# Performance work log

Hardware: AMD Instinct MI355X
Metric: run time of the kernel (lower is better)

Reference implementation:

```python
import jax, jax.numpy as jnp
import numpy as np

N_NODES = 100000
N_EDGES = 1600000
MAX_RADIUS = 3.0
NUM_BASIS = 3
SQRT2 = 2.0 ** 0.5
# e3nn soft_one_hot_linspace 'smooth_finite' prefactor
C_SMOOTH = 1.14136 * float(np.exp(2.0))


def _sus(x):
    # smooth unit step: exp(-1/x) for x>0 else 0 (NaN-safe for grad)
    safe = jnp.where(x > 0.0, x, 1.0)
    return jnp.where(x > 0.0, jnp.exp(-1.0 / safe), 0.0)


def radial_embed(d):
    # soft_one_hot_linspace(d, 0, max_radius, 3, basis='smooth_finite', cutoff=True) * sqrt(num_basis)
    values = jnp.linspace(0.0, MAX_RADIUS, NUM_BASIS + 2)[1:-1]  # [3]
    step = MAX_RADIUS / (NUM_BASIS + 1)
    diff = (d[:, None] - values) / step  # [E,3]
    y = C_SMOOTH * _sus(diff + 1.0) * _sus(1.0 - diff)
    return y * (NUM_BASIS ** 0.5)


def fcnet(x, w1, w2):
    # e3nn FullyConnectedNet([3,16,numel], relu): normalized weights, normalize2mom(relu)=sqrt(2)*relu
    h = SQRT2 * jax.nn.relu(x @ (w1 / w1.shape[0] ** 0.5))
    return h @ (w2 / w2.shape[0] ** 0.5)


def reference(pos, feat, edge_src, edge_dst, fc1_w1, fc1_w2, core_w1, core_w2, fc3_w1, fc3_w2, conv_w, conv_b):
    n = pos.shape[0]
    z = edge_src.shape[0] / n  # average num neighbors
    edge_vec = pos[edge_dst] - pos[edge_src]
    d = jnp.sqrt(jnp.sum(edge_vec * edge_vec, axis=1))  # edges are self-loop-free -> d > 0
    emb = radial_embed(d)  # [E,3]

    # NOTE on e3nn math: with input/mid/output parities all even and sh = 0e+1o+2e,
    # the only parity-allowed paths producing nonzero output are the 0e (scalar) paths,
    # which contract against Y_0 = 1 ('component' normalization). The 4x1e block of the
    # mid irreps is identically zero (no parity-allowed path ever populates it), so the
    # math below (scalar block only, with e3nn path weights) is exactly equivalent.
    def conv(x, w1, w2, mul_in, mul_out, path_w):
        # per-edge weights from radial MLP; keep the 0e->0e instruction block
        w = fcnet(emb, w1, w2)[:, : mul_in * mul_out].reshape(-1, mul_in, mul_out)
        msg = path_w * jnp.einsum('euw,eu->ew', w, x[edge_src])
        return jax.ops.segment_sum(msg, edge_dst, num_segments=n) / z ** 0.5

    x = conv(feat, fc1_w1, fc1_w2, 3, 4, (1.0 / 3.0) ** 0.5)  # tp1: fan_in 3*1 -> pw=1/sqrt(3)
    for i in range(3):
        x = conv(x, core_w1[i], core_w2[i], 4, 4, 0.5)  # tp2 0e path: pw=sqrt(1/4)
    x = conv(x, fc3_w1, fc3_w2, 4, 16, 0.5)  # tp3: pw=sqrt(1/4)
    # Conv1d(16, 2, 1) == pointwise linear
    return x @ conv_w.T + conv_b


def setup_inputs():
    key = jax.random.key(0)
    ks = jax.random.split(key, 12)
    pos = jax.random.uniform(ks[0], (N_NODES, 3), dtype=jnp.float32)  # unit box -> all edge lengths < max_radius
    feat = jax.random.normal(ks[1], (N_NODES, 3), dtype=jnp.float32)
    edge_src = jax.random.randint(ks[2], (N_EDGES,), 0, N_NODES, dtype=jnp.int32)
    off = jax.random.randint(ks[3], (N_EDGES,), 1, N_NODES, dtype=jnp.int32)
    edge_dst = ((edge_src + off) % N_NODES).astype(jnp.int32)  # radius_graph has no self-loops
    return {
        'pos': pos,
        'feat': feat,
        'edge_src': edge_src,
        'edge_dst': edge_dst,
        'fc1_w1': jax.random.normal(ks[4], (3, 16), jnp.float32),
        'fc1_w2': jax.random.normal(ks[5], (16, 12), jnp.float32),
        'core_w1': jax.random.normal(ks[6], (3, 3, 16), jnp.float32),
        'core_w2': jax.random.normal(ks[7], (3, 16, 48), jnp.float32),
        'fc3_w1': jax.random.normal(ks[8], (3, 16), jnp.float32),
        'fc3_w2': jax.random.normal(ks[9], (16, 64), jnp.float32),
        'conv_w': jax.random.normal(ks[10], (2, 16), jnp.float32) * 0.25,
        'conv_b': jax.random.normal(ks[11], (2,), jnp.float32) * 0.1,
    }
```

## Files before the change

kernel.cpp:

```cpp
#include <hip/hip_runtime.h>


#define BCAP 4608
#define NBMAX 400

__device__ __forceinline__ float sus_f(float x) {
    return x > 0.0f ? __expf(-1.0f / x) : 0.0f;
}

__device__ __forceinline__ float uload(const float* p) {
    return __uint_as_float(__builtin_amdgcn_readfirstlane(__float_as_uint(*p)));
}

__global__ __launch_bounds__(128) void k_prep_g(
    const float* __restrict__ w2, const float* __restrict__ cw,
    float* __restrict__ gbuf)
{
    int idx = threadIdx.x;
    int k = idx >> 3, u = (idx >> 1) & 3, c = idx & 1;
    float s = 0.0f;
    #pragma unroll
    for (int w = 0; w < 16; ++w)
        s = fmaf(w2[k * 64 + u * 16 + w], cw[c * 16 + w], s);
    gbuf[idx] = s;
}

__global__ __launch_bounds__(256) void k_bin(
    const int* __restrict__ src, const int* __restrict__ dst,
    const float* __restrict__ pos,
    int* __restrict__ gcur, float4* __restrict__ etmp,
    int nedges, int nb)
{
    __shared__ int cnt[NBMAX];
    __shared__ int gb[NBMAX];
    for (int b = threadIdx.x; b < nb; b += 256) cnt[b] = 0;
    __syncthreads();
    int base = blockIdx.x * 2048;
    int pk[8]; int bk[8]; short r[8];
    #pragma unroll
    for (int i = 0; i < 8; ++i) {
        int e = base + i * 256 + threadIdx.x;
        if (e < nedges) {
            int s = src[e], t = dst[e];
            int b = t >> 8;
            bk[i] = b;
            pk[i] = (s << 8) | (t & 255);
            r[i] = (short)atomicAdd(&cnt[b], 1);
        } else bk[i] = -1;
    }
    __syncthreads();
    for (int b = threadIdx.x; b < nb; b += 256) {
        int c = cnt[b];
        gb[b] = c > 0 ? atomicAdd(&gcur[b], c) : 0;
    }
    __syncthreads();
    const float C = 1.14136f * 7.3890560989306495f;
    #pragma unroll
    for (int i = 0; i < 8; ++i) {
        if (bk[i] < 0) continue;
        int p = gb[bk[i]] + (int)r[i];
        if (p >= BCAP) continue;
        int s = pk[i] >> 8;
        int t = (bk[i] << 8) | (pk[i] & 255);
        float dx = pos[3 * t + 0] - pos[3 * s + 0];
        float dy = pos[3 * t + 1] - pos[3 * s + 1];
        float dz = pos[3 * t + 2] - pos[3 * s + 2];
        float d = sqrtf(dx * dx + dy * dy + dz * dz);
        float e0, e1, e2;
        { float f = (d - 0.75f) * (1.0f / 0.75f);
          e0 = C * sus_f(f + 1.0f) * sus_f(1.0f - f); }
        { float f = (d - 1.50f) * (1.0f / 0.75f);
          e1 = C * sus_f(f + 1.0f) * sus_f(1.0f - f); }
        { float f = (d - 2.25f) * (1.0f / 0.75f);
          e2 = C * sus_f(f + 1.0f) * sus_f(1.0f - f); }
        etmp[(size_t)bk[i] * BCAP + p] =
            make_float4(__int_as_float(pk[i]), e0, e1, e2);
    }
}

__global__ __launch_bounds__(256) void k_build(
    const int* __restrict__ gcur, const float4* __restrict__ etmp,
    float4* __restrict__ ebuf, int2* __restrict__ offs2,
    int n, int nb)
{
    int b = blockIdx.x;
    int cnt = gcur[b]; if (cnt > BCAP) cnt = BCAP;

    __shared__ unsigned short rnk[BCAP];
    __shared__ int deg[256];
    __shared__ int loffs[256];

    const float4* tin = etmp + (size_t)b * BCAP;
    deg[threadIdx.x] = 0;
    __syncthreads();

    for (int j = threadIdx.x; j < cnt; j += 256) {
        int pkd = __float_as_int(tin[j].x);
        rnk[j] = (unsigned short)atomicAdd(&deg[pkd & 255], 1);
    }
    __syncthreads();

    {
        int t = threadIdx.x;
        int v = deg[t];
        loffs[t] = v; __syncthreads();
        for (int off = 1; off < 256; off <<= 1) {
            int val = (t >= off) ? loffs[t - off] : 0;
            __syncthreads();
            loffs[t] += val;
            __syncthreads();
        }
        int incl = loffs[t];
        __syncthreads();
        loffs[t] = incl - v;
        __syncthreads();
    }

    {
        int nid0 = b << 8;
        int nn = n - nid0; if (nn > 256) nn = 256;
        int t = threadIdx.x;
        if (t < nn) {
            int st = b * BCAP + loffs[t];
            offs2[nid0 + t] = make_int2(st, st + deg[t]);
        }
    }

    for (int j = threadIdx.x; j < cnt; j += 256) {
        float4 rec = tin[j];
        int pkd = __float_as_int(rec.x);
        int ln = pkd & 255;
        int slot = b * BCAP + loffs[ln] + (int)rnk[j];
        ebuf[slot] = make_float4(__int_as_float(pkd >> 8), rec.y, rec.z, rec.w);
    }
}


__global__ __launch_bounds__(256) void k_node_l1(
    const float* __restrict__ feat, const float4* __restrict__ edata,
    const int2* __restrict__ offs2,
    const float* __restrict__ w1, const float* __restrict__ w2,
    float* __restrict__ xout, int n)
{
    __shared__ float lw[16 * 20];
    if (threadIdx.x < 192) {
        int k = threadIdx.x / 12, r = threadIdx.x % 12;
        lw[k * 20 + r] = w2[k * 12 + r];
    }
    __syncthreads();

    int g = blockIdx.x * 256 + threadIdx.x;
    int nd = g >> 2;
    if (nd >= n) return;
    int t = g & 3;

    float w1r[3][16];
    #pragma unroll
    for (int j = 0; j < 3; ++j)
        #pragma unroll
        for (int k = 0; k < 16; ++k) w1r[j][k] = uload(&w1[j * 16 + k]);

    float O[16][3];
    #pragma unroll
    for (int k = 0; k < 16; ++k)
        #pragma unroll
        for (int u = 0; u < 3; ++u) O[k][u] = 0.0f;

    int2 se = offs2[nd];
    for (int e = se.x + t; e < se.y; e += 4) {
        float4 ed = edata[e];
        int s = __float_as_int(ed.x);
        float f0 = feat[3 * s + 0], f1 = feat[3 * s + 1], f2 = feat[3 * s + 2];
        #pragma unroll
        for (int k = 0; k < 16; ++k) {
            float a = fmaf(ed.y, w1r[0][k], fmaf(ed.z, w1r[1][k], ed.w * w1r[2][k]));
            float h = a > 0.0f ? a : 0.0f;
            O[k][0] = fmaf(h, f0, O[k][0]);
            O[k][1] = fmaf(h, f1, O[k][1]);
            O[k][2] = fmaf(h, f2, O[k][2]);
        }
    }

    float p0 = 0.f, p1 = 0.f, p2 = 0.f, p3 = 0.f;
    #pragma unroll
    for (int k = 0; k < 16; ++k)
        #pragma unroll
        for (int u = 0; u < 3; ++u) {
            const float4 q = *(const float4*)&lw[k * 20 + u * 4];
            float o = O[k][u];
            p0 = fmaf(o, q.x, p0); p1 = fmaf(o, q.y, p1);
            p2 = fmaf(o, q.z, p2); p3 = fmaf(o, q.w, p3);
        }
    p0 += __shfl_xor(p0, 1); p1 += __shfl_xor(p1, 1);
    p2 += __shfl_xor(p2, 1); p3 += __shfl_xor(p3, 1);
    p0 += __shfl_xor(p0, 2); p1 += __shfl_xor(p1, 2);
    p2 += __shfl_xor(p2, 2); p3 += __shfl_xor(p3, 2);
    if (t == 0) {
        const float S = 0.051031036307982884f;
        float4 o; o.x = p0 * S; o.y = p1 * S; o.z = p2 * S; o.w = p3 * S;
        ((float4*)xout)[nd] = o;
    }
}

__global__ __launch_bounds__(256) void k_node_core(
    const float4* __restrict__ xin, const float4* __restrict__ edata,
    const int2* __restrict__ offs2,
    const float* __restrict__ w1, const float* __restrict__ w2,
    float* __restrict__ xout, int n)
{
    __shared__ float lw[16 * 20];
    {
        int idx = threadIdx.x;
        int k = idx >> 4, r = idx & 15;
        lw[k * 20 + r] = w2[k * 48 + r];
    }
    __syncthreads();

    int g = blockIdx.x * 256 + threadIdx.x;
    int nd = g >> 2;
    if (nd >= n) return;
    int t = g & 3;

    float w1r[3][16];
    #pragma unroll
    for (int j = 0; j < 3; ++j)
        #pragma unroll
        for (int k = 0; k < 16; ++k) w1r[j][k] = uload(&w1[j * 16 + k]);

    float O[16][4];
    #pragma unroll
    for (int k = 0; k < 16; ++k)
        #pragma unroll
        for (int u = 0; u < 4; ++u) O[k][u] = 0.0f;

    int2 se = offs2[nd];
    for (int e = se.x + t; e < se.y; e += 4) {
        float4 ed = edata[e];
        int s = __float_as_int(ed.x);
        float4 x = xin[s];
        #pragma unroll
        for (int k = 0; k < 16; ++k) {
            float a = fmaf(ed.y, w1r[0][k], fmaf(ed.z, w1r[1][k], ed.w * w1r[2][k]));
            float h = a > 0.0f ? a : 0.0f;
            O[k][0] = fmaf(h, x.x, O[k][0]);
            O[k][1] = fmaf(h, x.y, O[k][1]);
            O[k][2] = fmaf(h, x.z, O[k][2]);
            O[k][3] = fmaf(h, x.w, O[k][3]);
        }
    }

    float p0 = 0.f, p1 = 0.f, p2 = 0.f, p3 = 0.f;
    #pragma unroll
    for (int k = 0; k < 16; ++k)
        #pragma unroll
        for (int u = 0; u < 4; ++u) {
            const float4 q = *(const float4*)&lw[k * 20 + u * 4];
            float o = O[k][u];
            p0 = fmaf(o, q.x, p0); p1 = fmaf(o, q.y, p1);
            p2 = fmaf(o, q.z, p2); p3 = fmaf(o, q.w, p3);
        }
    p0 += __shfl_xor(p0, 1); p1 += __shfl_xor(p1, 1);
    p2 += __shfl_xor(p2, 1); p3 += __shfl_xor(p3, 1);
    p0 += __shfl_xor(p0, 2); p1 += __shfl_xor(p1, 2);
    p2 += __shfl_xor(p2, 2); p3 += __shfl_xor(p3, 2);
    if (t == 0) {
        const float S = 0.04419417382415922f;
        float4 o; o.x = p0 * S; o.y = p1 * S; o.z = p2 * S; o.w = p3 * S;
        ((float4*)xout)[nd] = o;
    }
}

__global__ __launch_bounds__(256) void k_node_fc3_final(
    const float4* __restrict__ xin, const float4* __restrict__ edata,
    const int2* __restrict__ offs2,
    const float* __restrict__ w1, const float* __restrict__ gbuf,
    const float* __restrict__ cb,
    float* __restrict__ out, int n)
{
    __shared__ float lg[128];
    if (threadIdx.x < 128) lg[threadIdx.x] = gbuf[threadIdx.x];
    __syncthreads();

    int g = blockIdx.x * 256 + threadIdx.x;
    int nd = g >> 2;
    if (nd >= n) return;
    int t = g & 3;

    float w1r[3][16];
    #pragma unroll
    for (int j = 0; j < 3; ++j)
        #pragma unroll
        for (int k = 0; k < 16; ++k) w1r[j][k] = uload(&w1[j * 16 + k]);

    float O[16][4];
    #pragma unroll
    for (int k = 0; k < 16; ++k)
        #pragma unroll
        for (int u = 0; u < 4; ++u) O[k][u] = 0.0f;

    int2 se = offs2[nd];
    for (int e = se.x + t; e < se.y; e += 4) {
        float4 ed = edata[e];
        int s = __float_as_int(ed.x);
        float4 x = xin[s];
        #pragma unroll
        for (int k = 0; k < 16; ++k) {
            float a = fmaf(ed.y, w1r[0][k], fmaf(ed.z, w1r[1][k], ed.w * w1r[2][k]));
            float h = a > 0.0f ? a : 0.0f;
            O[k][0] = fmaf(h, x.x, O[k][0]);
            O[k][1] = fmaf(h, x.y, O[k][1]);
            O[k][2] = fmaf(h, x.z, O[k][2]);
            O[k][3] = fmaf(h, x.w, O[k][3]);
        }
    }

    float a0 = 0.f, a1 = 0.f;
    #pragma unroll
    for (int k = 0; k < 16; ++k)
        #pragma unroll
        for (int u = 0; u < 4; ++u) {
            float o = O[k][u];
            const float2 q = *(const float2*)&lg[(k * 4 + u) * 2];
            a0 = fmaf(o, q.x, a0);
            a1 = fmaf(o, q.y, a1);
        }
    a0 += __shfl_xor(a0, 1); a1 += __shfl_xor(a1, 1);
    a0 += __shfl_xor(a0, 2); a1 += __shfl_xor(a1, 2);
    if (t == 0) {
        const float S = 0.04419417382415922f;
        float2 o; o.x = fmaf(a0, S, cb[0]); o.y = fmaf(a1, S, cb[1]);
        ((float2*)out)[nd] = o;
    }
}


extern "C" void kernel_launch(void* const* d_in, const int* in_sizes, int n_in,
                              void* d_out, int out_size, void* d_ws, size_t ws_size,
                              hipStream_t stream) {
    const float* pos     = (const float*)d_in[0];
    const float* feat    = (const float*)d_in[1];
    const int*   esrc    = (const int*)d_in[2];
    const int*   edst    = (const int*)d_in[3];
    const float* fc1_w1  = (const float*)d_in[4];
    const float* fc1_w2  = (const float*)d_in[5];
    const float* core_w1 = (const float*)d_in[6];
    const float* core_w2 = (const float*)d_in[7];
    const float* fc3_w1  = (const float*)d_in[8];
    const float* fc3_w2  = (const float*)d_in[9];
    const float* conv_w  = (const float*)d_in[10];
    const float* conv_b  = (const float*)d_in[11];
    float* out = (float*)d_out;

    const int E = in_sizes[2];
    const int N = in_sizes[0] / 3;
    const int nb = (N + 255) >> 8;

    float4* ebuf = (float4*)d_ws;
    float4* etmp = ebuf + (size_t)nb * BCAP;
    float* xa = (float*)(etmp + (size_t)nb * BCAP);
    float* xb = xa + (size_t)4 * N;
    int2* offs2 = (int2*)(xb + (size_t)4 * N);
    int* gcur = (int*)(offs2 + N);
    float* gbuf = (float*)(gcur + ((nb + 3) & ~3));

    int g4 = (4 * N + 255) / 256;

    hipMemsetAsync(gcur, 0, (size_t)nb * sizeof(int), stream);
    k_prep_g<<<1, 128, 0, stream>>>(fc3_w2, conv_w, gbuf);
    k_bin<<<(E + 2047) / 2048, 256, 0, stream>>>(esrc, edst, pos, gcur,
                                                 etmp, E, nb);
    k_build<<<nb, 256, 0, stream>>>(gcur, etmp, ebuf, offs2, N, nb);

    k_node_l1<<<g4, 256, 0, stream>>>(feat, ebuf, offs2, fc1_w1, fc1_w2, xa, N);
    k_node_core<<<g4, 256, 0, stream>>>((const float4*)xa, ebuf, offs2,
                                        core_w1 + 0, core_w2 + 0, xb, N);
    k_node_core<<<g4, 256, 0, stream>>>((const float4*)xb, ebuf, offs2,
                                        core_w1 + 48, core_w2 + 768, xa, N);
    k_node_core<<<g4, 256, 0, stream>>>((const float4*)xa, ebuf, offs2,
                                        core_w1 + 96, core_w2 + 1536, xb, N);
    k_node_fc3_final<<<g4, 256, 0, stream>>>((const float4*)xb, ebuf, offs2,
                                             fc3_w1, gbuf, conv_b, out, N);
}
```

Measured before the change: 253.7 us.

## Bin packed edge indices only and compute radial embeddings in a separate pass

The binning kernel now writes only a packed 4-byte src/local-dst index per edge instead of a 16-byte float4 with embeddings, and loads src/dst with vectorized int4 reads of 8 consecutive edges per thread. The build kernel stages bucket indices in shared memory and scatters them into a CSR-ordered permutation in shared memory before writing them out coalesced. A new k_emb kernel then computes distances and smooth basis embeddings in final CSR order, which gives coalesced writes and dst-local pos reads. The aim is to cut the scattered 16-byte traffic through the temporary buffer. The cost is one extra kernel launch and an extra index buffer pass, and within-node edge order becomes atomic-dependent, so float summation order can vary between runs.

Result: faster. 240.2 us (-5.3%).

```diff
diff --git a/kernel.cpp b/kernel.cpp
--- a/kernel.cpp
+++ b/kernel.cpp
@@ -27,26 +27,45 @@
 
 __global__ __launch_bounds__(256) void k_bin(
     const int* __restrict__ src, const int* __restrict__ dst,
-    const float* __restrict__ pos,
-    int* __restrict__ gcur, float4* __restrict__ etmp,
+    int* __restrict__ gcur, int* __restrict__ ptmp,
     int nedges, int nb)
 {
     __shared__ int cnt[NBMAX];
     __shared__ int gb[NBMAX];
     for (int b = threadIdx.x; b < nb; b += 256) cnt[b] = 0;
     __syncthreads();
-    int base = blockIdx.x * 2048;
+
+    int base = blockIdx.x * 2048 + threadIdx.x * 8;
     int pk[8]; int bk[8]; short r[8];
-    #pragma unroll
-    for (int i = 0; i < 8; ++i) {
-        int e = base + i * 256 + threadIdx.x;
-        if (e < nedges) {
-            int s = src[e], t = dst[e];
-            int b = t >> 8;
+    int ss[8], dd[8];
+    if (base + 7 < nedges) {
+        int4 s0 = *(const int4*)&src[base];
+        int4 s1 = *(const int4*)&src[base + 4];
+        int4 d0 = *(const int4*)&dst[base];
+        int4 d1 = *(const int4*)&dst[base + 4];
+        ss[0]=s0.x; ss[1]=s0.y; ss[2]=s0.z; ss[3]=s0.w;
+        ss[4]=s1.x; ss[5]=s1.y; ss[6]=s1.z; ss[7]=s1.w;
+        dd[0]=d0.x; dd[1]=d0.y; dd[2]=d0.z; dd[3]=d0.w;
+        dd[4]=d1.x; dd[5]=d1.y; dd[6]=d1.z; dd[7]=d1.w;
+        #pragma unroll
+        for (int i = 0; i < 8; ++i) {
+            int b = dd[i] >> 8;
             bk[i] = b;
-            pk[i] = (s << 8) | (t & 255);
+            pk[i] = (ss[i] << 8) | (dd[i] & 255);
             r[i] = (short)atomicAdd(&cnt[b], 1);
-        } else bk[i] = -1;
+        }
+    } else {
+        #pragma unroll
+        for (int i = 0; i < 8; ++i) {
+            int e = base + i;
+            if (e < nedges) {
+                int s = src[e], t = dst[e];
+                int b = t >> 8;
+                bk[i] = b;
+                pk[i] = (s << 8) | (t & 255);
+                r[i] = (short)atomicAdd(&cnt[b], 1);
+            } else bk[i] = -1;
+        }
     }
     __syncthreads();
     for (int b = threadIdx.x; b < nb; b += 256) {
@@ -54,50 +73,37 @@
         gb[b] = c > 0 ? atomicAdd(&gcur[b], c) : 0;
     }
     __syncthreads();
-    const float C = 1.14136f * 7.3890560989306495f;
     #pragma unroll
     for (int i = 0; i < 8; ++i) {
-        if (bk[i] < 0) continue;
-        int p = gb[bk[i]] + (int)r[i];
-        if (p >= BCAP) continue;
-        int s = pk[i] >> 8;
-        int t = (bk[i] << 8) | (pk[i] & 255);
-        float dx = pos[3 * t + 0] - pos[3 * s + 0];
-        float dy = pos[3 * t + 1] - pos[3 * s + 1];
-        float dz = pos[3 * t + 2] - pos[3 * s + 2];
-        float d = sqrtf(dx * dx + dy * dy + dz * dz);
-        float e0, e1, e2;
-        { float f = (d - 0.75f) * (1.0f / 0.75f);
-          e0 = C * sus_f(f + 1.0f) * sus_f(1.0f - f); }
-        { float f = (d - 1.50f) * (1.0f / 0.75f);
-          e1 = C * sus_f(f + 1.0f) * sus_f(1.0f - f); }
-        { float f = (d - 2.25f) * (1.0f / 0.75f);
-          e2 = C * sus_f(f + 1.0f) * sus_f(1.0f - f); }
-        etmp[(size_t)bk[i] * BCAP + p] =
-            make_float4(__int_as_float(pk[i]), e0, e1, e2);
+        if (bk[i] >= 0) {
+            int p = gb[bk[i]] + (int)r[i];
+            if (p < BCAP)
+                ptmp[bk[i] * BCAP + p] = pk[i];
+        }
     }
 }
 
 __global__ __launch_bounds__(256) void k_build(
-    const int* __restrict__ gcur, const float4* __restrict__ etmp,
-    float4* __restrict__ ebuf, int2* __restrict__ offs2,
+    const int* __restrict__ gcur, const int* __restrict__ ptmp,
+    int* __restrict__ pidx, int2* __restrict__ offs2,
     int n, int nb)
 {
     int b = blockIdx.x;
     int cnt = gcur[b]; if (cnt > BCAP) cnt = BCAP;
 
-    __shared__ unsigned short rnk[BCAP];
+    __shared__ int stage[BCAP];
+    __shared__ int perm[BCAP];
     __shared__ int deg[256];
     __shared__ int loffs[256];
-
-    const float4* tin = etmp + (size_t)b * BCAP;
+    __shared__ int cur[256];
+
+    const int* tin = ptmp + b * BCAP;
+    for (int j = threadIdx.x; j < cnt; j += 256) stage[j] = tin[j];
     deg[threadIdx.x] = 0;
     __syncthreads();
 
-    for (int j = threadIdx.x; j < cnt; j += 256) {
-        int pkd = __float_as_int(tin[j].x);
-        rnk[j] = (unsigned short)atomicAdd(&deg[pkd & 255], 1);
-    }
+    for (int j = threadIdx.x; j < cnt; j += 256)
+        atomicAdd(&deg[stage[j] & 255], 1);
     __syncthreads();
 
     {
@@ -113,6 +119,7 @@
         int incl = loffs[t];
         __syncthreads();
         loffs[t] = incl - v;
+        cur[t] = incl - v;
         __syncthreads();
     }
 
@@ -127,12 +134,38 @@
     }
 
     for (int j = threadIdx.x; j < cnt; j += 256) {
-        float4 rec = tin[j];
-        int pkd = __float_as_int(rec.x);
-        int ln = pkd & 255;
-        int slot = b * BCAP + loffs[ln] + (int)rnk[j];
-        ebuf[slot] = make_float4(__int_as_float(pkd >> 8), rec.y, rec.z, rec.w);
-    }
+        int pkd = stage[j];
+        perm[atomicAdd(&cur[pkd & 255], 1)] = pkd;
+    }
+    __syncthreads();
+
+    int* tout = pidx + b * BCAP;
+    for (int j = threadIdx.x; j < cnt; j += 256) tout[j] = perm[j];
+}
+
+__global__ __launch_bounds__(256) void k_emb(
+    const float* __restrict__ pos, const int* __restrict__ gcur,
+    const int* __restrict__ pidx, float4* __restrict__ ebuf)
+{
+    int b = blockIdx.y;
+    int j = blockIdx.x * 256 + threadIdx.x;
+    if (j >= gcur[b]) return;
+    int pkd = pidx[b * BCAP + j];
+    int s = pkd >> 8;
+    int t = (b << 8) | (pkd & 255);
+    float dx = pos[3 * t + 0] - pos[3 * s + 0];
+    float dy = pos[3 * t + 1] - pos[3 * s + 1];
+    float dz = pos[3 * t + 2] - pos[3 * s + 2];
+    float d = sqrtf(dx * dx + dy * dy + dz * dz);
+    const float C = 1.14136f * 7.3890560989306495f;
+    float e0, e1, e2;
+    { float f = (d - 0.75f) * (1.0f / 0.75f);
+      e0 = C * sus_f(f + 1.0f) * sus_f(1.0f - f); }
+    { float f = (d - 1.50f) * (1.0f / 0.75f);
+      e1 = C * sus_f(f + 1.0f) * sus_f(1.0f - f); }
+    { float f = (d - 2.25f) * (1.0f / 0.75f);
+      e2 = C * sus_f(f + 1.0f) * sus_f(1.0f - f); }
+    ebuf[(size_t)b * BCAP + j] = make_float4(__int_as_float(s), e0, e1, e2);
 }
 
 
@@ -356,20 +389,24 @@
     const int nb = (N + 255) >> 8;
 
     float4* ebuf = (float4*)d_ws;
-    float4* etmp = ebuf + (size_t)nb * BCAP;
-    float* xa = (float*)(etmp + (size_t)nb * BCAP);
-    float* xb = xa + (size_t)4 * N;
+    int* ptmp  = (int*)(ebuf + (size_t)nb * BCAP);
+    int* pidx  = ptmp + (size_t)nb * BCAP;
+    float* xa  = (float*)(pidx + (size_t)nb * BCAP);
+    float* xb  = xa + (size_t)4 * N;
     int2* offs2 = (int2*)(xb + (size_t)4 * N);
-    int* gcur = (int*)(offs2 + N);
+    int* gcur  = (int*)(offs2 + N);
     float* gbuf = (float*)(gcur + ((nb + 3) & ~3));
 
     int g4 = (4 * N + 255) / 256;
 
     hipMemsetAsync(gcur, 0, (size_t)nb * sizeof(int), stream);
     k_prep_g<<<1, 128, 0, stream>>>(fc3_w2, conv_w, gbuf);
-    k_bin<<<(E + 2047) / 2048, 256, 0, stream>>>(esrc, edst, pos, gcur,
-                                                 etmp, E, nb);
-    k_build<<<nb, 256, 0, stream>>>(gcur, etmp, ebuf, offs2, N, nb);
+    k_bin<<<(E + 2047) / 2048, 256, 0, stream>>>(esrc, edst, gcur, ptmp, E, nb);
+    k_build<<<nb, 256, 0, stream>>>(gcur, ptmp, pidx, offs2, N, nb);
+    {
+        dim3 eg(BCAP / 256, nb);
+        k_emb<<<eg, 256, 0, stream>>>(pos, gcur, pidx, ebuf);
+    }
 
     k_node_l1<<<g4, 256, 0, stream>>>(feat, ebuf, offs2, fc1_w1, fc1_w2, xa, N);
     k_node_core<<<g4, 256, 0, stream>>>((const float4*)xa, ebuf, offs2,
```
